# Optimization experiments

Hardware: AMD Instinct MI355X
Metric: run time of the kernel (lower is better)

Reference implementation:

```python
import jax, jax.numpy as jnp
import numpy as np

D = 256   # dim = vis_dim = key_channels = value_channels = audio_dim
BT = 64   # batch*time
H = 64
W = 64
L = 32    # audio length

_CONV_NAMES = ["vis_project", "av", "vv", "vo", "ao", "vs_key", "vs_q1", "vs_q2",
               "as_key", "as_q1", "as_q2", "outconv", "aoc"]


def _conv1(x, w, b):
    # pointwise Conv1d: x [B,C,Lx], w [O,C], b [O]
    return jnp.einsum('oc,bcl->bol', w, x) + b[None, :, None]


def _inorm(x, eps=1e-5):
    # InstanceNorm1d (affine=False): normalize over last (spatial) axis
    m = jnp.mean(x, axis=-1, keepdims=True)
    v = jnp.var(x, axis=-1, keepdims=True)
    return (x - m) * jax.lax.rsqrt(v + eps)


def _gelu(x):
    return jax.nn.gelu(x, approximate=False)


def setup_inputs() -> dict:
    key = jax.random.key(0)
    ks = jax.random.split(key, 40)
    inp = {
        "x": jax.random.normal(ks[0], (BT, D, H, W), jnp.float32),
        "audio": jax.random.normal(ks[1], (BT, D, L), jnp.float32),
        "audio_mask": jnp.ones((BT, L, 1), jnp.float32),
    }
    for i, n in enumerate(_CONV_NAMES):
        inp[n + "_w"] = jax.random.normal(ks[3 + 2 * i], (D, D), jnp.float32) * 0.05
        inp[n + "_b"] = jax.random.normal(ks[4 + 2 * i], (D,), jnp.float32) * 0.01
    inp["gate_w1"] = jax.random.normal(ks[30], (D, D), jnp.float32) * 0.05
    inp["gate_w2"] = jax.random.normal(ks[31], (D, D), jnp.float32) * 0.05
    inp["vis_weight"] = jnp.ones((1,), jnp.float32)
    inp["audio_weight"] = jnp.ones((1,), jnp.float32)
    return inp


def reference(x, audio, audio_mask,
              vis_project_w, vis_project_b, av_w, av_b, vv_w, vv_b, vo_w, vo_b,
              ao_w, ao_b, vs_key_w, vs_key_b, vs_q1_w, vs_q1_b, vs_q2_w, vs_q2_b,
              as_key_w, as_key_b, as_q1_w, as_q1_b, as_q2_w, as_q2_b,
              outconv_w, outconv_b, aoc_w, aoc_b, gate_w1, gate_w2,
              vis_weight, audio_weight):
    bt, c, h, w = x.shape
    hw = h * w
    xf = x.reshape(bt, c, hw)                       # [BT,C,HW] (channels-first tokens)
    scale = float(D) ** -0.5                         # key_channels ** -0.5
    maskT = jnp.swapaxes(audio_mask, 1, 2)           # [BT,1,L]

    # vis_project (Conv1d 1x1 + GELU)
    vis = _gelu(_conv1(xf, vis_project_w, vis_project_b))       # [BT,C,HW]

    # ---- AV_Interaction ----
    audio_value = _conv1(audio, av_w, av_b) * maskT              # [BT,C,L]

    # Visual_Sim (kernel=1 -> unfold is identity)
    q1 = _inorm(_conv1(xf, vs_q1_w, vs_q1_b))                    # [BT,C,HW]
    q = _inorm(_conv1(q1, vs_q2_w, vs_q2_b))                     # [BT,C,HW]
    k = _conv1(audio, vs_key_w, vs_key_b) * maskT                # [BT,C,L]
    sim_v = jnp.einsum('bch,bcl->bhl', q, k) * scale             # [BT,HW,L]
    sim_v = sim_v + (10000.0 * maskT - 10000.0)                  # mask keys
    sim_v = jax.nn.softmax(sim_v, axis=-1)
    vw = jax.nn.softmax(vis_weight)[0]                           # softmax over size-1 -> 1.0
    vis_out = jnp.einsum('bhl,bcl->bhc', sim_v * vw, audio_value)  # [BT,HW,C]
    vis_out = _inorm(_conv1(jnp.swapaxes(vis_out, 1, 2), vo_w, vo_b))  # [BT,C,HW]

    # Audio_Sim (kernel=(1,1) -> pad/unfold identity)
    aq = _conv1(_conv1(audio, as_q1_w, as_q1_b), as_q2_w, as_q2_b)  # [BT,C,L]
    ak = _inorm(_conv1(xf, as_key_w, as_key_b))                     # [BT,C,HW]
    aqT = jnp.swapaxes(aq, 1, 2) * audio_mask                       # [BT,L,C]
    sim_a = jnp.einsum('blc,bch->blh', aqT, ak) * scale             # [BT,L,HW]
    sim_a = sim_a + (10000.0 * audio_mask - 10000.0)                # mask query rows
    sim_a = jax.nn.softmax(sim_a, axis=-1)
    aw = jax.nn.softmax(audio_weight)[0]
    vis_value = _inorm(_conv1(xf, vv_w, vv_b))                      # [BT,C,HW]
    audio_o = jnp.einsum('blh,bch->blc', sim_a * aw, vis_value)     # [BT,L,C]
    audio_res = _conv1(jnp.swapaxes(audio_o, 1, 2), ao_w, ao_b)     # [BT,C,L]

    # ---- Dual fusion: vis * vis_weight_map, out_conv ----
    vis = _gelu(_conv1(vis * vis_out, outconv_w, outconv_b))        # [BT,C,HW]
    vis_res = jnp.swapaxes(vis, 1, 2)                               # [BT,HW,C]

    # ---- DAM block: gated residual + audio residual ----
    gate = jnp.tanh(jax.nn.relu(vis_res @ gate_w1.T) @ gate_w2.T)   # [BT,HW,C]
    x_tok = jnp.swapaxes(xf, 1, 2) + gate * vis_res                 # [BT,HW,C]
    x_out = jnp.swapaxes(x_tok, 1, 2).reshape(bt, c, h, w)
    audio_out = audio + _gelu(_conv1(audio_res, aoc_w, aoc_b))      # [BT,C,L]
    return (x_out, audio_out)
```

## Files before the change

### kernel.cpp

```cpp
#include <hip/hip_runtime.h>
#include <math.h>

#define BT 64
#define CH 256
#define HW 4096
#define AL 32
#define SCALE 0.0625f

typedef unsigned short ushort_t;
typedef __bf16 bf16x8 __attribute__((ext_vector_type(8)));
typedef short  short8 __attribute__((ext_vector_type(8)));
typedef float  f32x4  __attribute__((ext_vector_type(4)));

__device__ __forceinline__ float gelu_f(float x){
    return 0.5f*x*(1.0f+erff(x*0.70710678118654752f));
}
__device__ __forceinline__ ushort_t f2bf(float f){
    unsigned int u = __builtin_bit_cast(unsigned int, f);
    u += 0x7fffu + ((u>>16)&1u);
    return (ushort_t)(u>>16);
}
__device__ __forceinline__ float bf2f(ushort_t h){
    unsigned int u = ((unsigned int)h)<<16;
    return __builtin_bit_cast(float, u);
}

#define GLOAD_LDS16(gp, lp) __builtin_amdgcn_global_load_lds( \
    (const __attribute__((address_space(1))) unsigned int*)(gp), \
    (__attribute__((address_space(3))) unsigned int*)(lp), 16, 0, 0)

template<int EPI, int TOUT, int WSTAT>
__global__ __launch_bounds__(256,2)
void gemm_mfma_kernel(const ushort_t* __restrict__ Wb, const float* __restrict__ bias,
                      const ushort_t* __restrict__ Xt, float* __restrict__ Out,
                      ushort_t* __restrict__ OutB,
                      const float* __restrict__ E1, const float* __restrict__ E2,
                      float* __restrict__ St)
{
    __shared__ ushort_t sW[128*32];
    __shared__ ushort_t sX[128*32];
    const int b  = blockIdx.z;
    const int o0 = blockIdx.y*128, p0 = blockIdx.x*128;
    const int tid = threadIdx.x, lane = tid & 63, w = tid >> 6;
    const int wm = w >> 1, wn = w & 1;
    const int rr = lane >> 2;
    const int kk8 = (lane & 3) * 8;

    f32x4 acc[4][4] = {};

    for (int k0 = 0; k0 < CH; k0 += 32) {
        #pragma unroll
        for (int j = 0; j < 2; ++j) {
            const ushort_t* gw = Wb + (size_t)(o0 + w*32 + j*16 + rr)*CH + k0 + kk8;
            GLOAD_LDS16(gw, sW + (size_t)w*1024 + j*512);
        }
        #pragma unroll
        for (int j = 0; j < 2; ++j) {
            const ushort_t* gx = Xt + ((size_t)b*HW + p0 + w*32 + j*16 + rr)*CH + k0 + kk8;
            GLOAD_LDS16(gx, sX + (size_t)w*1024 + j*512);
        }
        __syncthreads();
        bf16x8 af[4], bfr[4];
        #pragma unroll
        for (int mt = 0; mt < 4; ++mt) {
            short8 raw = *(const short8*)(sW + (size_t)(wm*64 + mt*16 + (lane&15))*32 + (lane>>4)*8);
            af[mt] = __builtin_bit_cast(bf16x8, raw);
        }
        #pragma unroll
        for (int nt = 0; nt < 4; ++nt) {
            short8 raw = *(const short8*)(sX + (size_t)(wn*64 + nt*16 + (lane&15))*32 + (lane>>4)*8);
            bfr[nt] = __builtin_bit_cast(bf16x8, raw);
        }
        #pragma unroll
        for (int mt = 0; mt < 4; ++mt)
            #pragma unroll
            for (int nt = 0; nt < 4; ++nt)
                acc[mt][nt] = __builtin_amdgcn_mfma_f32_16x16x32_bf16(af[mt], bfr[nt], acc[mt][nt], 0, 0, 0);
        __syncthreads();
    }

    const int pcol = lane & 15, quad = lane >> 4;
    const size_t obase = (size_t)b*CH*HW;
    if (TOUT == 0) {
        #pragma unroll
        for (int mt = 0; mt < 4; ++mt) {
            #pragma unroll
            for (int r = 0; r < 4; ++r) {
                const int o = o0 + wm*64 + mt*16 + quad*4 + r;
                const float bv = bias ? bias[o] : 0.0f;
                #pragma unroll
                for (int nt = 0; nt < 4; ++nt) {
                    const int p = p0 + wn*64 + nt*16 + pcol;
                    float v = acc[mt][nt][r] + bv;
                    if (EPI == 1) v = gelu_f(v);
                    if (EPI == 2) v = fmaxf(v, 0.0f);
                    if (EPI == 3) {
                        const size_t idx = obase + (size_t)o*HW + p;
                        v = E1[idx] + tanhf(v)*E2[idx];
                    }
                    Out[obase + (size_t)o*HW + p] = v;
                }
            }
        }
    } else if (TOUT == 1) {
        #pragma unroll
        for (int mt = 0; mt < 4; ++mt) {
            const int ob = o0 + wm*64 + mt*16 + quad*4;
            #pragma unroll
            for (int nt = 0; nt < 4; ++nt) {
                const int p = p0 + wn*64 + nt*16 + pcol;
                ushort4 u;
                float v0 = acc[mt][nt][0] + (bias ? bias[ob+0] : 0.f);
                float v1 = acc[mt][nt][1] + (bias ? bias[ob+1] : 0.f);
                float v2 = acc[mt][nt][2] + (bias ? bias[ob+2] : 0.f);
                float v3 = acc[mt][nt][3] + (bias ? bias[ob+3] : 0.f);
                if (EPI == 1) { v0=gelu_f(v0); v1=gelu_f(v1); v2=gelu_f(v2); v3=gelu_f(v3); }
                if (EPI == 2) { v0=fmaxf(v0,0.f); v1=fmaxf(v1,0.f); v2=fmaxf(v2,0.f); v3=fmaxf(v3,0.f); }
                u.x=f2bf(v0); u.y=f2bf(v1); u.z=f2bf(v2); u.w=f2bf(v3);
                *(ushort4*)(OutB + ((size_t)b*HW + p)*CH + ob) = u;
            }
        }
    } else {
        #pragma unroll
        for (int mt = 0; mt < 4; ++mt) {
            const int ob = o0 + wm*64 + mt*16 + quad*4;
            #pragma unroll
            for (int nt = 0; nt < 4; ++nt) {
                const int p = p0 + wn*64 + nt*16 + pcol;
                float v[4];
                #pragma unroll
                for (int r = 0; r < 4; ++r) {
                    float t = acc[mt][nt][r] + (bias ? bias[ob+r] : 0.f);
                    if (EPI == 1) t = gelu_f(t);
                    if (EPI == 2) t = fmaxf(t, 0.f);
                    v[r] = t;
                    Out[obase + (size_t)(ob+r)*HW + p] = t;
                }
                ushort4 u;
                u.x=f2bf(v[0]); u.y=f2bf(v[1]); u.z=f2bf(v[2]); u.w=f2bf(v[3]);
                *(ushort4*)(OutB + ((size_t)b*HW + p)*CH + ob) = u;
            }
        }
    }

    if (WSTAT) {
        float s1[4][4], s2[4][4];
        #pragma unroll
        for (int mt = 0; mt < 4; ++mt) {
            #pragma unroll
            for (int r = 0; r < 4; ++r) {
                const int o = o0 + wm*64 + mt*16 + quad*4 + r;
                const float bv = bias ? bias[o] : 0.0f;
                float a = 0.f, q = 0.f;
                #pragma unroll
                for (int nt = 0; nt < 4; ++nt) {
                    const float v = acc[mt][nt][r] + bv;
                    a += v; q += v*v;
                }
                #pragma unroll
                for (int off = 1; off < 16; off <<= 1) {
                    a += __shfl_xor(a, off);
                    q += __shfl_xor(q, off);
                }
                s1[mt][r] = a; s2[mt][r] = q;
            }
        }
        float* red = (float*)sW;
        __syncthreads();
        if (wn == 0 && pcol == 0) {
            #pragma unroll
            for (int mt = 0; mt < 4; ++mt)
                #pragma unroll
                for (int r = 0; r < 4; ++r) {
                    const int ol = wm*64 + mt*16 + quad*4 + r;
                    red[ol*2] = s1[mt][r]; red[ol*2+1] = s2[mt][r];
                }
        }
        __syncthreads();
        if (wn == 1 && pcol == 0) {
            #pragma unroll
            for (int mt = 0; mt < 4; ++mt)
                #pragma unroll
                for (int r = 0; r < 4; ++r) {
                    const int ol = wm*64 + mt*16 + quad*4 + r;
                    const int o = o0 + ol;
                    atomicAdd(&St[((size_t)b*CH + o)*2],   red[ol*2]   + s1[mt][r]);
                    atomicAdd(&St[((size_t)b*CH + o)*2+1], red[ol*2+1] + s2[mt][r]);
                }
        }
    }
}

__global__ __launch_bounds__(256)
void zero_kernel(float* __restrict__ p)
{
    p[blockIdx.x*256 + threadIdx.x] = 0.f;
}

__global__ __launch_bounds__(256)
void stats_finalize_kernel(float* __restrict__ St)
{
    const int row = blockIdx.x*256 + threadIdx.x;
    const float s1 = St[(size_t)row*2], s2 = St[(size_t)row*2+1];
    const float mean = s1 * (1.0f/HW);
    const float var  = s2 * (1.0f/HW) - mean*mean;
    St[(size_t)row*2]   = mean;
    St[(size_t)row*2+1] = rsqrtf(var + 1e-5f);
}

template<int MODE>
__global__ __launch_bounds__(256)
void transpose_bf16_kernel(const float* __restrict__ Xa, const ushort_t* __restrict__ Mul,
                           const float* __restrict__ St, ushort_t* __restrict__ Out)
{
    __shared__ float sT[32][33];
    const int b = blockIdx.z, c0 = blockIdx.y*32, p0 = blockIdx.x*32;
    const int tid = threadIdx.x;
    {
        const int cr = tid >> 3, pq = (tid & 7)*4;
        float4 v = *(const float4*)(Xa + ((size_t)b*CH + c0 + cr)*HW + p0 + pq);
        if (MODE >= 1) {
            const float m = St[((size_t)b*CH + c0 + cr)*2];
            const float r = St[((size_t)b*CH + c0 + cr)*2+1];
            v.x = (v.x-m)*r; v.y = (v.y-m)*r; v.z = (v.z-m)*r; v.w = (v.w-m)*r;
        }
        sT[cr][pq+0]=v.x; sT[cr][pq+1]=v.y; sT[cr][pq+2]=v.z; sT[cr][pq+3]=v.w;
    }
    __syncthreads();
    {
        const int pr = tid >> 3, cq = (tid & 7)*4;
        const size_t oidx = ((size_t)b*HW + p0 + pr)*CH + c0 + cq;
        float v0 = sT[cq+0][pr], v1 = sT[cq+1][pr], v2 = sT[cq+2][pr], v3 = sT[cq+3][pr];
        if (MODE == 2) {
            const ushort4 m = *(const ushort4*)(Mul + oidx);
            v0 *= bf2f(m.x); v1 *= bf2f(m.y); v2 *= bf2f(m.z); v3 *= bf2f(m.w);
        }
        ushort4 u; u.x=f2bf(v0); u.y=f2bf(v1); u.z=f2bf(v2); u.w=f2bf(v3);
        *(ushort4*)(Out + oidx) = u;
    }
}

__global__ __launch_bounds__(256)
void wconv_kernel(const float* w0, const float* w1, const float* w2, const float* w3,
                  const float* w4, const float* w5, const float* w6, const float* w7,
                  const float* w8, ushort_t* __restrict__ Wb)
{
    const float* src;
    switch (blockIdx.y) {
        case 0: src=w0; break; case 1: src=w1; break; case 2: src=w2; break;
        case 3: src=w3; break; case 4: src=w4; break; case 5: src=w5; break;
        case 6: src=w6; break; case 7: src=w7; break; default: src=w8; break;
    }
    const int i = (blockIdx.x*256 + threadIdx.x)*4;
    const float4 v = *(const float4*)(src + i);
    ushort4 u; u.x=f2bf(v.x); u.y=f2bf(v.y); u.z=f2bf(v.z); u.w=f2bf(v.w);
    *(ushort4*)(Wb + (size_t)blockIdx.y*65536 + i) = u;
}

template<int EPI, int TR>
__global__ __launch_bounds__(256)
void conv_l_kernel(const float* __restrict__ W, const float* __restrict__ bias,
                   const float* __restrict__ X, float* __restrict__ Out,
                   const float* __restrict__ Mask, const float* __restrict__ Resid,
                   const float* __restrict__ St)
{
    const int b = blockIdx.x;
    const int o = blockIdx.y*8 + (threadIdx.x>>5);
    const int l = threadIdx.x & 31;
    const float* xb = X + (size_t)b*CH*AL + l;
    const float* wr = W + (size_t)o*CH;
    float acc = bias ? bias[o] : 0.0f;
    #pragma unroll 8
    for (int c=0;c<CH;++c) acc = fmaf(wr[c], xb[(size_t)c*AL], acc);
    if (EPI==1) acc *= Mask[b*AL + l];
    if (EPI==4) acc *= Mask[b*AL + l] * St[((size_t)b*CH + o)*2+1] * SCALE;
    if (EPI==2) {
        const size_t oi = (size_t)b*CH*AL + (size_t)o*AL + l;
        acc = Resid[oi] + gelu_f(acc);
    }
    if (TR == 0) Out[(size_t)b*CH*AL + (size_t)o*AL + l] = acc;
    else         Out[((size_t)b*AL + l)*CH + o] = acc;
}

__global__ __launch_bounds__(256)
void lbias_kernel(const float* __restrict__ Kn, const float* __restrict__ St,
                  float* __restrict__ Lb)
{
    const int b = blockIdx.x, tid = threadIdx.x;
    const int l = tid & 31, g = tid >> 5;
    float s = 0.f;
    #pragma unroll 8
    for (int cc=0; cc<32; ++cc){
        const int c = g*32 + cc;
        s += St[((size_t)b*CH + c)*2] * Kn[((size_t)b*CH + c)*AL + l];
    }
    __shared__ float red[8][32];
    red[g][l] = s;
    __syncthreads();
    if (tid < 32){
        float t = 0.f;
        #pragma unroll
        for (int gg=0; gg<8; ++gg) t += red[gg][tid];
        Lb[b*AL + tid] = -t;
    }
}

__global__ __launch_bounds__(256,2)
void attn_v_kernel(const float* __restrict__ Q, const float* __restrict__ Kn,
                   const float* __restrict__ AVt, const float* __restrict__ Lb,
                   const float* __restrict__ Mask, ushort_t* __restrict__ OutB)
{
    __shared__ float smemf[20480];
    float*    sKn  = smemf;
    ushort_t* sOut = (ushort_t*)smemf;
    ushort_t* sPb  = (ushort_t*)(smemf + 8192);
    float*    sAV  = smemf + 12288;

    const int b  = blockIdx.y;
    const int p0 = blockIdx.x * 256;
    const int tid = threadIdx.x, lane = tid & 63, w = tid >> 6;
    const int pg = lane >> 2;
    const int lq = lane & 3;

    #pragma unroll
    for (int ii=0; ii<8; ++ii){
        const int fi = ii*256 + tid;
        *(f32x4*)&sKn[fi*4] = *(const f32x4*)(Kn + (size_t)b*CH*AL + (size_t)fi*4);
        *(f32x4*)&sAV[fi*4] = *(const f32x4*)(AVt + (size_t)b*AL*CH + (size_t)fi*4);
    }
    float bias[8];
    #pragma unroll
    for (int j=0;j<8;++j){
        const int l = lq*8 + j;
        bias[j] = Lb[b*AL + l] + 10000.f*Mask[b*AL + l] - 10000.f;
    }
    __syncthreads();

    const float* Qb = Q + (size_t)b*CH*HW + p0 + w*64 + pg*4;
    float s[4][8] = {};
    {
        f32x4 qa[8], qb2[8];
        #pragma unroll
        for (int kk=0;kk<8;++kk) qa[kk] = *(const f32x4*)(Qb + (size_t)kk*HW);
        for (int kc = 0; kc < 32; kc += 2){
            #pragma unroll
            for (int kk=0;kk<8;++kk) qb2[kk] = *(const f32x4*)(Qb + (size_t)((kc+1)*8+kk)*HW);
            #pragma unroll
            for (int kk=0;kk<8;++kk){
                const int c = kc*8 + kk;
                const f32x4 kn0 = *(const f32x4*)&sKn[c*32 + lq*8];
                const f32x4 kn1 = *(const f32x4*)&sKn[c*32 + lq*8 + 4];
                #pragma unroll
                for (int i=0;i<4;++i){
                    s[i][0]=fmaf(qa[kk][i],kn0[0],s[i][0]); s[i][1]=fmaf(qa[kk][i],kn0[1],s[i][1]);
                    s[i][2]=fmaf(qa[kk][i],kn0[2],s[i][2]); s[i][3]=fmaf(qa[kk][i],kn0[3],s[i][3]);
                    s[i][4]=fmaf(qa[kk][i],kn1[0],s[i][4]); s[i][5]=fmaf(qa[kk][i],kn1[1],s[i][5]);
                    s[i][6]=fmaf(qa[kk][i],kn1[2],s[i][6]); s[i][7]=fmaf(qa[kk][i],kn1[3],s[i][7]);
                }
            }
            if (kc+2 < 32){
                #pragma unroll
                for (int kk=0;kk<8;++kk) qa[kk] = *(const f32x4*)(Qb + (size_t)((kc+2)*8+kk)*HW);
            }
            #pragma unroll
            for (int kk=0;kk<8;++kk){
                const int c = (kc+1)*8 + kk;
                const f32x4 kn0 = *(const f32x4*)&sKn[c*32 + lq*8];
                const f32x4 kn1 = *(const f32x4*)&sKn[c*32 + lq*8 + 4];
                #pragma unroll
                for (int i=0;i<4;++i){
                    s[i][0]=fmaf(qb2[kk][i],kn0[0],s[i][0]); s[i][1]=fmaf(qb2[kk][i],kn0[1],s[i][1]);
                    s[i][2]=fmaf(qb2[kk][i],kn0[2],s[i][2]); s[i][3]=fmaf(qb2[kk][i],kn0[3],s[i][3]);
                    s[i][4]=fmaf(qb2[kk][i],kn1[0],s[i][4]); s[i][5]=fmaf(qb2[kk][i],kn1[1],s[i][5]);
                    s[i][6]=fmaf(qb2[kk][i],kn1[2],s[i][6]); s[i][7]=fmaf(qb2[kk][i],kn1[3],s[i][7]);
                }
            }
        }
    }

    #pragma unroll
    for (int i=0;i<4;++i){
        #pragma unroll
        for (int j=0;j<8;++j) s[i][j] += bias[j];
        float m = s[i][0];
        #pragma unroll
        for (int j=1;j<8;++j) m = fmaxf(m, s[i][j]);
        m = fmaxf(m, __shfl_xor(m, 1));
        m = fmaxf(m, __shfl_xor(m, 2));
        float z = 0.f;
        #pragma unroll
        for (int j=0;j<8;++j){ s[i][j] = expf(s[i][j]-m); z += s[i][j]; }
        z += __shfl_xor(z, 1);
        z += __shfl_xor(z, 2);
        const float rz = 1.f/z;
        #pragma unroll
        for (int j=0;j<8;++j) s[i][j] *= rz;
    }

    {
        const int tok = w*64 + pg*4;
        #pragma unroll
        for (int j=0;j<8;++j){
            const int l = lq*8 + j;
            unsigned u01 = (unsigned)f2bf(s[0][j]) | ((unsigned)f2bf(s[1][j])<<16);
            unsigned u23 = (unsigned)f2bf(s[2][j]) | ((unsigned)f2bf(s[3][j])<<16);
            *(unsigned*)&sPb[l*256 + tok]     = u01;
            *(unsigned*)&sPb[l*256 + tok + 2] = u23;
        }
    }
    __syncthreads();

    const int tokL = tid >> 2;
    const int cq   = tid & 3;
    for (int t0 = 0; t0 < 4; ++t0){
        const int tok = t0*64 + tokL;
        float acc[8][8] = {};
        for (int k=0;k<32;++k){
            const float pv = bf2f(sPb[k*256 + tok]);
            #pragma unroll
            for (int ch=0;ch<8;++ch){
                const f32x4 a0 = *(const f32x4*)&sAV[k*256 + ch*32 + cq*8];
                const f32x4 a1 = *(const f32x4*)&sAV[k*256 + ch*32 + cq*8 + 4];
                acc[ch][0]=fmaf(pv,a0[0],acc[ch][0]); acc[ch][1]=fmaf(pv,a0[1],acc[ch][1]);
                acc[ch][2]=fmaf(pv,a0[2],acc[ch][2]); acc[ch][3]=fmaf(pv,a0[3],acc[ch][3]);
                acc[ch][4]=fmaf(pv,a1[0],acc[ch][4]); acc[ch][5]=fmaf(pv,a1[1],acc[ch][5]);
                acc[ch][6]=fmaf(pv,a1[2],acc[ch][6]); acc[ch][7]=fmaf(pv,a1[3],acc[ch][7]);
            }
        }
        #pragma unroll
        for (int ch=0;ch<8;++ch){
            short8 u;
            #pragma unroll
            for (int j=0;j<8;++j) u[j] = (short)f2bf(acc[ch][j]);
            const int chunk = (ch*4 + cq) ^ (tokL & 7);
            *(short8*)&sOut[tokL*256 + chunk*8] = u;
        }
        __syncthreads();
        {
            ushort_t* Ob = OutB + ((size_t)b*HW + p0 + t0*64)*CH;
            const int chunk = tid & 31;
            #pragma unroll
            for (int ss=0;ss<8;++ss){
                const int row = ss*8 + (tid>>5);
                short8 v = *(const short8*)&sOut[row*256 + ((chunk ^ (row&7))*8)];
                *(short8*)(Ob + (size_t)row*CH + chunk*8) = v;
            }
        }
        __syncthreads();
    }
}

__global__ __launch_bounds__(256)
void sima_raw_kernel(const float* __restrict__ AQ, const float* __restrict__ AK,
                     const float* __restrict__ Mask, const float* __restrict__ St,
                     float* __restrict__ Sraw)
{
    __shared__ float sAQ[CH*AL];
    const int b = blockIdx.y;
    const int p = blockIdx.x*256 + threadIdx.x;
    const int tid = threadIdx.x;
    #pragma unroll
    for (int i=0;i<32;++i){
        const int idx = tid + 256*i;
        sAQ[idx] = AQ[(size_t)b*CH*AL + idx] * Mask[b*AL + (idx&31)] * SCALE
                 * St[((size_t)b*CH + (idx>>5))*2+1];
    }
    __syncthreads();
    float s[32];
    #pragma unroll
    for (int l=0;l<32;++l) s[l]=0.f;
    const float* akb = AK + (size_t)b*CH*HW + p;
    for (int c=0;c<CH;++c){
        const float a = akb[(size_t)c*HW];
        const float* qr = &sAQ[c*32];
        #pragma unroll
        for (int l=0;l<32;++l) s[l] = fmaf(qr[l], a, s[l]);
    }
    float* outp = Sraw + (size_t)b*AL*HW + p;
    #pragma unroll
    for (int l=0;l<32;++l) outp[(size_t)l*HW] = s[l];
}

__global__ __launch_bounds__(256)
void sima_stats_kernel(const float* __restrict__ Sraw, float2* __restrict__ Stats)
{
    const size_t base = (size_t)blockIdx.x * HW;
    const int tid = threadIdx.x;
    float v[16];
    #pragma unroll
    for (int i=0;i<4;++i){
        const float4 t = *(const float4*)(Sraw + base + tid*4 + i*1024);
        v[i*4+0]=t.x; v[i*4+1]=t.y; v[i*4+2]=t.z; v[i*4+3]=t.w;
    }
    float m = v[0];
    #pragma unroll
    for (int i=1;i<16;++i) m = fmaxf(m, v[i]);
    #pragma unroll
    for (int off=1; off<64; off<<=1) m = fmaxf(m, __shfl_xor(m, off));
    __shared__ float rm[4], rz[4];
    if ((tid&63)==0) rm[tid>>6]=m;
    __syncthreads();
    m = fmaxf(fmaxf(rm[0],rm[1]), fmaxf(rm[2],rm[3]));
    float z=0.f;
    #pragma unroll
    for (int i=0;i<16;++i) z += expf(v[i]-m);
    #pragma unroll
    for (int off=1; off<64; off<<=1) z += __shfl_xor(z, off);
    if ((tid&63)==0) rz[tid>>6]=z;
    __syncthreads();
    if (tid==0) Stats[blockIdx.x] = make_float2(m, 1.0f/(rz[0]+rz[1]+rz[2]+rz[3]));
}

__global__ __launch_bounds__(256)
void sima_pv_kernel(const float* __restrict__ Sraw, const float2* __restrict__ SmStats,
                    const float* __restrict__ VV, const float* __restrict__ ChSt,
                    float* __restrict__ AO)
{
    __shared__ float sA[32*33];
    __shared__ float sB[64*36];
    __shared__ float sM[32], sR[32];
    const int b  = blockIdx.x >> 2;
    const int c0 = (blockIdx.x & 3) * 64;
    const int tid = threadIdx.x;
    if (tid < 32){
        const float2 st = SmStats[b*AL + tid];
        sM[tid] = st.x; sR[tid] = st.y;
    }
    __syncthreads();
    const int lh = tid & 15;
    const int cq = tid >> 4;
    const int lr = tid >> 3, k4 = (tid & 7) * 4;
    float acc[2][4] = {{0.f,0.f,0.f,0.f},{0.f,0.f,0.f,0.f}};
    for (int p0=0; p0<HW; p0+=32){
        {
            const float4 t = *(const float4*)(Sraw + ((size_t)b*AL + lr)*HW + p0 + k4);
            const float mm = sM[lr], rr2 = sR[lr];
            sA[lr*33 + k4+0] = expf(t.x-mm)*rr2;
            sA[lr*33 + k4+1] = expf(t.y-mm)*rr2;
            sA[lr*33 + k4+2] = expf(t.z-mm)*rr2;
            sA[lr*33 + k4+3] = expf(t.w-mm)*rr2;
        }
        #pragma unroll
        for (int i=0;i<2;++i){
            const int cc = (tid>>3) + 32*i;
            *(float4*)&sB[cc*36 + k4] = *(const float4*)(VV + ((size_t)b*CH + c0 + cc)*HW + p0 + k4);
        }
        __syncthreads();
        #pragma unroll
        for (int kk=0;kk<32;++kk){
            const float a0 = sA[lh*33 + kk];
            const float a1 = sA[(lh+16)*33 + kk];
            #pragma unroll
            for (int j=0;j<4;++j){
                const float bb = sB[(cq*4+j)*36 + kk];
                acc[0][j] = fmaf(a0, bb, acc[0][j]);
                acc[1][j] = fmaf(a1, bb, acc[1][j]);
            }
        }
        __syncthreads();
    }
    #pragma unroll
    for (int j=0;j<4;++j){
        const int c = c0 + cq*4 + j;
        const float m0 = ChSt[((size_t)b*CH + c)*2];
        const float r0 = ChSt[((size_t)b*CH + c)*2+1];
        AO[((size_t)b*CH + c)*AL + lh]      = (acc[0][j]-m0)*r0;
        AO[((size_t)b*CH + c)*AL + lh + 16] = (acc[1][j]-m0)*r0;
    }
}

extern "C" void kernel_launch(void* const* d_in, const int* in_sizes, int n_in,
                              void* d_out, int out_size, void* d_ws, size_t ws_size,
                              hipStream_t stream)
{
    (void)in_sizes; (void)n_in; (void)out_size; (void)ws_size;
    const float* x     = (const float*)d_in[0];
    const float* audio = (const float*)d_in[1];
    const float* amask = (const float*)d_in[2];
    const float* vis_project_w = (const float*)d_in[3];
    const float* vis_project_b = (const float*)d_in[4];
    const float* av_w = (const float*)d_in[5];
    const float* av_b = (const float*)d_in[6];
    const float* vv_w = (const float*)d_in[7];
    const float* vv_b = (const float*)d_in[8];
    const float* vo_w = (const float*)d_in[9];
    const float* vo_b = (const float*)d_in[10];
    const float* ao_w = (const float*)d_in[11];
    const float* ao_b = (const float*)d_in[12];
    const float* vs_key_w = (const float*)d_in[13];
    const float* vs_key_b = (const float*)d_in[14];
    const float* vs_q1_w = (const float*)d_in[15];
    const float* vs_q1_b = (const float*)d_in[16];
    const float* vs_q2_w = (const float*)d_in[17];
    const float* vs_q2_b = (const float*)d_in[18];
    const float* as_key_w = (const float*)d_in[19];
    const float* as_key_b = (const float*)d_in[20];
    const float* as_q1_w = (const float*)d_in[21];
    const float* as_q1_b = (const float*)d_in[22];
    const float* as_q2_w = (const float*)d_in[23];
    const float* as_q2_b = (const float*)d_in[24];
    const float* outconv_w = (const float*)d_in[25];
    const float* outconv_b = (const float*)d_in[26];
    const float* aoc_w = (const float*)d_in[27];
    const float* aoc_b = (const float*)d_in[28];
    const float* gate_w1 = (const float*)d_in[29];
    const float* gate_w2 = (const float*)d_in[30];

    float* out_x = (float*)d_out;
    float* out_a = out_x + (size_t)BT*CH*HW;
    float* B     = out_x;

    const size_t BIG = (size_t)BT*CH*HW;
    ushort_t* Xt   = (ushort_t*)d_ws;
    ushort_t* VISB = Xt + BIG;
    float*  A     = (float*)(VISB + BIG);
    float*  SIMA  = A + BIG;
    float2* STATS = (float2*)(SIMA + (size_t)BT*AL*HW);
    float*  S0 = (float*)(STATS + BT*AL);
    float*  S1 = S0 + (size_t)BT*CH*AL;
    float*  S2 = S1 + (size_t)BT*CH*AL;
    float*  S3 = S2 + (size_t)BT*CH*AL;
    float*  S4 = S3 + (size_t)BT*CH*AL;
    ushort_t* Wb = (ushort_t*)(S4 + (size_t)BT*CH*AL);
    float*  SA = (float*)(Wb + (size_t)9*65536);
    float*  SB = SA + (size_t)2*BT*CH;
    float*  LB = SB + (size_t)2*BT*CH;

    dim3 b256(256);
    dim3 gW(64, 9);
    dim3 gL(BT, CH/8);
    dim3 gT(HW/32, CH/32, BT);
    dim3 gG(HW/128, CH/128, BT);
    dim3 gAttnV(HW/256, BT);
    dim3 gSimA(HW/256, BT);
    dim3 gZ(2*BT*CH/256);
    dim3 gF(BT*CH/256);

    #define WSLOT(i) (Wb + (size_t)(i)*65536)
    hipLaunchKernelGGL(wconv_kernel, gW, b256, 0, stream,
                       vs_q1_w, as_key_w, vv_w, vis_project_w, vs_q2_w, vo_w, outconv_w, gate_w1, gate_w2, Wb);
    hipLaunchKernelGGL((conv_l_kernel<1,1>), gL, b256, 0, stream, av_w, av_b, audio, S0, amask, nullptr, nullptr);
    hipLaunchKernelGGL((conv_l_kernel<0,0>), gL, b256, 0, stream, as_q1_w, as_q1_b, audio, S3, nullptr, nullptr, nullptr);
    hipLaunchKernelGGL((conv_l_kernel<0,0>), gL, b256, 0, stream, as_q2_w, as_q2_b, S3, S2, nullptr, nullptr, nullptr);
    hipLaunchKernelGGL((transpose_bf16_kernel<0>), gT, b256, 0, stream, x, nullptr, nullptr, Xt);
    hipLaunchKernelGGL(zero_kernel, gZ, b256, 0, stream, SA);
    hipLaunchKernelGGL((gemm_mfma_kernel<0,0,1>), gG, b256, 0, stream, WSLOT(0), vs_q1_b, Xt, A, nullptr, nullptr, nullptr, SA);
    hipLaunchKernelGGL(stats_finalize_kernel, gF, b256, 0, stream, SA);
    hipLaunchKernelGGL(zero_kernel, gZ, b256, 0, stream, SB);
    hipLaunchKernelGGL((gemm_mfma_kernel<0,0,1>), gG, b256, 0, stream, WSLOT(1), as_key_b, Xt, B, nullptr, nullptr, nullptr, SB);
    hipLaunchKernelGGL(stats_finalize_kernel, gF, b256, 0, stream, SB);
    hipLaunchKernelGGL(sima_raw_kernel, gSimA, b256, 0, stream, S2, B, amask, SB, SIMA);
    hipLaunchKernelGGL(sima_stats_kernel, dim3(BT*AL), b256, 0, stream, SIMA, STATS);
    hipLaunchKernelGGL(zero_kernel, gZ, b256, 0, stream, SB);
    hipLaunchKernelGGL((gemm_mfma_kernel<0,0,1>), gG, b256, 0, stream, WSLOT(2), vv_b, Xt, B, nullptr, nullptr, nullptr, SB);
    hipLaunchKernelGGL(stats_finalize_kernel, gF, b256, 0, stream, SB);
    hipLaunchKernelGGL(sima_pv_kernel, dim3(BT*4), b256, 0, stream, SIMA, STATS, B, SB, S4);
    hipLaunchKernelGGL((conv_l_kernel<0,0>), gL, b256, 0, stream, ao_w, ao_b, S4, S3, nullptr, nullptr, nullptr);
    hipLaunchKernelGGL((conv_l_kernel<2,0>), gL, b256, 0, stream, aoc_w, aoc_b, S3, out_a, nullptr, audio, nullptr);
    hipLaunchKernelGGL((gemm_mfma_kernel<1,1,0>), gG, b256, 0, stream, WSLOT(3), vis_project_b, Xt, nullptr, VISB, nullptr, nullptr, nullptr);
    hipLaunchKernelGGL((transpose_bf16_kernel<1>), gT, b256, 0, stream, A, nullptr, SA, Xt);
    hipLaunchKernelGGL(zero_kernel, gZ, b256, 0, stream, SA);
    hipLaunchKernelGGL((gemm_mfma_kernel<0,0,1>), gG, b256, 0, stream, WSLOT(4), vs_q2_b, Xt, B, nullptr, nullptr, nullptr, SA);
    hipLaunchKernelGGL(stats_finalize_kernel, gF, b256, 0, stream, SA);
    hipLaunchKernelGGL((conv_l_kernel<4,0>), gL, b256, 0, stream, vs_key_w, vs_key_b, audio, S1, amask, nullptr, SA);
    hipLaunchKernelGGL(lbias_kernel, dim3(BT), b256, 0, stream, S1, SA, LB);
    hipLaunchKernelGGL(attn_v_kernel, gAttnV, b256, 0, stream, B, S1, S0, LB, amask, Xt);
    hipLaunchKernelGGL(zero_kernel, gZ, b256, 0, stream, SA);
    hipLaunchKernelGGL((gemm_mfma_kernel<0,0,1>), gG, b256, 0, stream, WSLOT(5), vo_b, Xt, B, nullptr, nullptr, nullptr, SA);
    hipLaunchKernelGGL(stats_finalize_kernel, gF, b256, 0, stream, SA);
    hipLaunchKernelGGL((transpose_bf16_kernel<2>), gT, b256, 0, stream, B, VISB, SA, Xt);
    hipLaunchKernelGGL((gemm_mfma_kernel<1,2,0>), gG, b256, 0, stream, WSLOT(6), outconv_b, Xt, A, VISB, nullptr, nullptr, nullptr);
    hipLaunchKernelGGL((gemm_mfma_kernel<2,1,0>), gG, b256, 0, stream, WSLOT(7), nullptr, VISB, nullptr, Xt, nullptr, nullptr, nullptr);
    hipLaunchKernelGGL((gemm_mfma_kernel<3,0,0>), gG, b256, 0, stream, WSLOT(8), nullptr, Xt, out_x, nullptr, x, A, nullptr);
    #undef WSLOT
}
```

Baseline: 2.716 ms.

## Double-buffer GEMM LDS tiles with XOR-swizzled layout and raise occupancy bound

The bf16 MFMA GEMM kernel now keeps two LDS stages for the weight and activation tiles. The next K-slice is prefetched with global_load_lds while MFMAs run on the current one, and only one barrier is left per iteration. The 16-byte chunk layout inside each LDS row is XOR-swizzled on both write and read to reduce bank conflicts, and launch bounds go from 2 to 3 blocks per SM. This doubles LDS use per block and tightens the register budget, which could cause spills or limit the occupancy actually reached.

```diff
diff --git a/kernel.cpp b/kernel.cpp
--- a/kernel.cpp
+++ b/kernel.cpp
@@ -30,45 +30,57 @@
     (__attribute__((address_space(3))) unsigned int*)(lp), 16, 0, 0)
 
 template<int EPI, int TOUT, int WSTAT>
-__global__ __launch_bounds__(256,2)
+__global__ __launch_bounds__(256,3)
 void gemm_mfma_kernel(const ushort_t* __restrict__ Wb, const float* __restrict__ bias,
                       const ushort_t* __restrict__ Xt, float* __restrict__ Out,
                       ushort_t* __restrict__ OutB,
                       const float* __restrict__ E1, const float* __restrict__ E2,
                       float* __restrict__ St)
 {
-    __shared__ ushort_t sW[128*32];
-    __shared__ ushort_t sX[128*32];
+    __shared__ ushort_t sW[2][128*32];
+    __shared__ ushort_t sX[2][128*32];
     const int b  = blockIdx.z;
     const int o0 = blockIdx.y*128, p0 = blockIdx.x*128;
     const int tid = threadIdx.x, lane = tid & 63, w = tid >> 6;
     const int wm = w >> 1, wn = w & 1;
-    const int rr = lane >> 2;
-    const int kk8 = (lane & 3) * 8;
+    const int rr  = lane >> 2;
+    const int csw = ((lane & 3) ^ ((lane >> 3) & 3)) * 8;
+
+    const ushort_t* gwb = Wb + (size_t)(o0 + w*32)*CH;
+    const ushort_t* gxb = Xt + ((size_t)b*HW + p0 + w*32)*CH;
 
     f32x4 acc[4][4] = {};
 
+    #pragma unroll
+    for (int j = 0; j < 2; ++j)
+        GLOAD_LDS16(gwb + (size_t)(j*16 + rr)*CH + csw, &sW[0][w*1024 + j*512]);
+    #pragma unroll
+    for (int j = 0; j < 2; ++j)
+        GLOAD_LDS16(gxb + (size_t)(j*16 + rr)*CH + csw, &sX[0][w*1024 + j*512]);
+    __syncthreads();
+
+    const int rchunk = ((lane >> 4) ^ ((lane >> 1) & 3)) * 8;
+
+    int cur = 0;
     for (int k0 = 0; k0 < CH; k0 += 32) {
-        #pragma unroll
-        for (int j = 0; j < 2; ++j) {
-            const ushort_t* gw = Wb + (size_t)(o0 + w*32 + j*16 + rr)*CH + k0 + kk8;
-            GLOAD_LDS16(gw, sW + (size_t)w*1024 + j*512);
-        }
-        #pragma unroll
-        for (int j = 0; j < 2; ++j) {
-            const ushort_t* gx = Xt + ((size_t)b*HW + p0 + w*32 + j*16 + rr)*CH + k0 + kk8;
-            GLOAD_LDS16(gx, sX + (size_t)w*1024 + j*512);
-        }
-        __syncthreads();
+        if (k0 + 32 < CH) {
+            const int nxt = cur ^ 1;
+            #pragma unroll
+            for (int j = 0; j < 2; ++j)
+                GLOAD_LDS16(gwb + (size_t)(j*16 + rr)*CH + k0 + 32 + csw, &sW[nxt][w*1024 + j*512]);
+            #pragma unroll
+            for (int j = 0; j < 2; ++j)
+                GLOAD_LDS16(gxb + (size_t)(j*16 + rr)*CH + k0 + 32 + csw, &sX[nxt][w*1024 + j*512]);
+        }
         bf16x8 af[4], bfr[4];
         #pragma unroll
         for (int mt = 0; mt < 4; ++mt) {
-            short8 raw = *(const short8*)(sW + (size_t)(wm*64 + mt*16 + (lane&15))*32 + (lane>>4)*8);
+            short8 raw = *(const short8*)(&sW[cur][(wm*64 + mt*16 + (lane&15))*32 + rchunk]);
             af[mt] = __builtin_bit_cast(bf16x8, raw);
         }
         #pragma unroll
         for (int nt = 0; nt < 4; ++nt) {
-            short8 raw = *(const short8*)(sX + (size_t)(wn*64 + nt*16 + (lane&15))*32 + (lane>>4)*8);
+            short8 raw = *(const short8*)(&sX[cur][(wn*64 + nt*16 + (lane&15))*32 + rchunk]);
             bfr[nt] = __builtin_bit_cast(bf16x8, raw);
         }
         #pragma unroll
@@ -77,6 +89,7 @@
             for (int nt = 0; nt < 4; ++nt)
                 acc[mt][nt] = __builtin_amdgcn_mfma_f32_16x16x32_bf16(af[mt], bfr[nt], acc[mt][nt], 0, 0, 0);
         __syncthreads();
+        cur ^= 1;
     }
 
     const int pcol = lane & 15, quad = lane >> 4;
```

Result: slower. 2.798 ms (+3.0%).
